# Performance work log

Measured on AMD Instinct MI355X. Metric: run time of the kernel, lower is better.

## Reference

```python
import jax, jax.numpy as jnp
import numpy as np


def setup_inputs() -> dict:
    key = jax.random.key(0)
    ks = jax.random.split(key, 6)
    B, F, C = 2048, 512, 64
    t_feat = jax.random.normal(ks[0], (B, F), dtype=jnp.float32)
    f_feat = jax.random.normal(ks[1], (B, F), dtype=jnp.float32)
    # proj Linear(F*F -> C); scale like torch default init (~1/sqrt(fan_in))
    W_proj = jax.random.normal(ks[2], (C, F * F), dtype=jnp.float32) / np.sqrt(F * F)
    b_proj = jnp.zeros((C,), dtype=jnp.float32)
    W1 = jax.random.normal(ks[3], (32, C), dtype=jnp.float32) / np.sqrt(C)
    b1 = jnp.zeros((32,), dtype=jnp.float32)
    W2 = jax.random.normal(ks[4], (1, 32), dtype=jnp.float32) / np.sqrt(32)
    b2 = jnp.zeros((1,), dtype=jnp.float32)
    return {"t_feat": t_feat, "f_feat": f_feat, "W_proj": W_proj, "b_proj": b_proj,
            "W1": W1, "b1": b1, "W2": W2, "b2": b2}


def reference(t_feat, f_feat, W_proj, b_proj, W1, b1, W2, b2):
    B, F = t_feat.shape
    C = W_proj.shape[0]
    # corr[b,i,j] = t[b,i] * f[b,j]; proj = corr_flat @ W_proj.T + b_proj.
    # Equivalent bilinear form computed WITHOUT materializing the (B,F,F) outer product:
    Wr = W_proj.reshape(C, F, F)            # W_proj[c, i*F + j] -> Wr[c,i,j]
    tmp = jnp.einsum('bi,cij->bcj', t_feat, Wr)   # (B, C, F)
    proj = jnp.einsum('bcj,bj->bc', tmp, f_feat) + b_proj  # (B, C)
    h = jax.nn.relu(proj)
    # GRL is identity in forward
    h2 = jax.nn.relu(h @ W1.T + b1)          # (B, 32)
    logit = h2 @ W2.T + b2                   # (B, 1)
    return logit
```

## Files before the change

kernel.cpp:

```cpp
#include <hip/hip_runtime.h>
#include <hip/hip_bf16.h>
#include <stdint.h>

#define BATCH 2048
#define FDIM 512
#define CDIM 64

typedef unsigned short ushort_t;
typedef __attribute__((ext_vector_type(8))) short short8;
typedef __attribute__((ext_vector_type(4))) float f32x4;

__device__ __forceinline__ ushort_t f2bf(float x) {
    union { float f; uint32_t u; } v; v.f = x;
    uint32_t u = v.u;
    uint32_t r = u + 0x7FFFu + ((u >> 16) & 1u);
    return (ushort_t)(r >> 16);
}

__global__ void convert_kernel(const float* __restrict__ src, ushort_t* __restrict__ dst) {
    int idx = blockIdx.x * 256 + threadIdx.x;
    float4 v = ((const float4*)src)[idx];
    ushort_t p[4] = { f2bf(v.x), f2bf(v.y), f2bf(v.z), f2bf(v.w) };
    *(uint2*)&dst[idx * 4] = *(uint2*)p;
}

#define AS3(p) ((__attribute__((address_space(3))) void*)(p))
#define AS1(p) ((const __attribute__((address_space(1))) void*)(p))

__launch_bounds__(256, 2)
__global__ void gemm_fused_kernel(const ushort_t* __restrict__ f16,
                                  const ushort_t* __restrict__ Wb,
                                  const float* __restrict__ t_feat,
                                  float* __restrict__ part) {
    __shared__ ushort_t As[128 * 32];
    __shared__ ushort_t Bs[128 * 32];
    __shared__ float scratch[256];

    const int tid  = threadIdx.x;
    const int wave = tid >> 6;
    const int lane = tid & 63;
    const int l15  = lane & 15;
    const int lg   = lane >> 4;

    const int b0 = blockIdx.x * 128;
    const int n0 = blockIdx.y * 128;

    const int m_base = (wave >> 1) * 64;
    const int nh     = wave & 1;
    const int n_base = nh * 64;

    f32x4 acc[4][4];
    #pragma unroll
    for (int mi = 0; mi < 4; mi++)
        #pragma unroll
        for (int ni = 0; ni < 4; ni++)
            acc[mi][ni] = (f32x4){0.f, 0.f, 0.f, 0.f};

    const int p    = tid >> 2;
    const int cph  = tid & 3;
    const int cg   = cph ^ ((p >> 1) & 3);
    const int nrot = ((p & 15) << 2) | (p >> 4);

    const ushort_t* gA0 = f16 + (size_t)(b0 + p) * FDIM + cg * 8;
    const ushort_t* gA1 = f16 + (size_t)(b0 + 64 + p) * FDIM + cg * 8;
    const ushort_t* gB0 = Wb + (size_t)(n0 + nrot) * FDIM + cg * 8;
    const ushort_t* gB1 = Wb + (size_t)(n0 + 64 + nrot) * FDIM + cg * 8;

    for (int k0 = 0; k0 < FDIM; k0 += 32) {
        __builtin_amdgcn_global_load_lds(AS1(gA0 + k0), AS3(&As[0 * 2048 + wave * 512]), 16, 0, 0);
        __builtin_amdgcn_global_load_lds(AS1(gA1 + k0), AS3(&As[1 * 2048 + wave * 512]), 16, 0, 0);
        __builtin_amdgcn_global_load_lds(AS1(gB0 + k0), AS3(&Bs[0 * 2048 + wave * 512]), 16, 0, 0);
        __builtin_amdgcn_global_load_lds(AS1(gB1 + k0), AS3(&Bs[1 * 2048 + wave * 512]), 16, 0, 0);
        __syncthreads();

        short8 a[4], b[4];
        #pragma unroll
        for (int mi = 0; mi < 4; mi++) {
            int r = m_base + mi * 16 + l15;
            a[mi] = *(const short8*)&As[r * 32 + (lg ^ ((r >> 1) & 3)) * 8];
        }
        #pragma unroll
        for (int ni = 0; ni < 4; ni++) {
            int q = n_base + ni * 16 + l15;
            b[ni] = *(const short8*)&Bs[q * 32 + (lg ^ ((q >> 1) & 3)) * 8];
        }

        #pragma unroll
        for (int mi = 0; mi < 4; mi++)
            #pragma unroll
            for (int ni = 0; ni < 4; ni++)
                acc[mi][ni] = __builtin_amdgcn_mfma_f32_16x16x32_bf16(a[mi], b[ni], acc[mi][ni], 0, 0, 0);

        __syncthreads();
    }

    const int c  = n0 >> 9;
    const int iq = (n0 >> 7) & 3;
    const int i_base = (n0 & 511) + n_base + l15 * 4;

    #pragma unroll
    for (int mi = 0; mi < 4; mi++) {
        #pragma unroll
        for (int r = 0; r < 4; r++) {
            int b_idx = b0 + m_base + mi * 16 + lg * 4 + r;
            const float4 tv = *(const float4*)&t_feat[(size_t)b_idx * FDIM + i_base];
            float s = acc[mi][0][r] * tv.x + acc[mi][1][r] * tv.y
                    + acc[mi][2][r] * tv.z + acc[mi][3][r] * tv.w;
            s += __shfl_xor(s, 1, 64);
            s += __shfl_xor(s, 2, 64);
            s += __shfl_xor(s, 4, 64);
            s += __shfl_xor(s, 8, 64);
            if (l15 == 0)
                scratch[(m_base + mi * 16 + lg * 4 + r) * 2 + nh] = s;
        }
    }
    __syncthreads();
    if (tid < 128) {
        float v = scratch[tid * 2] + scratch[tid * 2 + 1];
        part[(((size_t)(b0 + tid)) * 64 + c) * 4 + iq] = v;
    }
}

__global__ void mlp_kernel(const float* __restrict__ part,
                           const float* __restrict__ b_proj,
                           const float* __restrict__ W1, const float* __restrict__ b1,
                           const float* __restrict__ W2, const float* __restrict__ b2,
                           float* __restrict__ out) {
    int b = blockIdx.x * 64 + threadIdx.x;
    float h[64];
    const float4* p4 = (const float4*)&part[(size_t)b * 256];
    #pragma unroll
    for (int c = 0; c < 64; c++) {
        float4 v = p4[c];
        float s = v.x + v.y + v.z + v.w + b_proj[c];
        h[c] = s > 0.f ? s : 0.f;
    }
    float logit = b2[0];
    for (int o = 0; o < 32; o++) {
        float s = b1[o];
        #pragma unroll
        for (int c = 0; c < 64; c++) s += h[c] * W1[o * 64 + c];
        logit += (s > 0.f ? s : 0.f) * W2[o];
    }
    out[b] = logit;
}

extern "C" void kernel_launch(void* const* d_in, const int* in_sizes, int n_in,
                              void* d_out, int out_size, void* d_ws, size_t ws_size,
                              hipStream_t stream) {
    const float* t_feat = (const float*)d_in[0];
    const float* f_feat = (const float*)d_in[1];
    const float* W_proj = (const float*)d_in[2];
    const float* b_proj = (const float*)d_in[3];
    const float* W1     = (const float*)d_in[4];
    const float* b1     = (const float*)d_in[5];
    const float* W2     = (const float*)d_in[6];
    const float* b2     = (const float*)d_in[7];
    float* out = (float*)d_out;

    uint8_t* ws = (uint8_t*)d_ws;
    ushort_t* Wb   = (ushort_t*)(ws);
    ushort_t* f16  = (ushort_t*)(ws + 33554432);
    float*    part = (float*)(ws + 33554432 + 2097152);

    convert_kernel<<<dim3((CDIM * FDIM * FDIM) / 1024), dim3(256), 0, stream>>>(W_proj, Wb);
    convert_kernel<<<dim3((BATCH * FDIM) / 1024), dim3(256), 0, stream>>>(f_feat, f16);

    gemm_fused_kernel<<<dim3(BATCH / 128, (CDIM * FDIM) / 128), dim3(256), 0, stream>>>(
        f16, Wb, t_feat, part);

    mlp_kernel<<<dim3(BATCH / 64), dim3(64), 0, stream>>>(part, b_proj, W1, b1, W2, b2, out);
}
```

Measured before the change: 231.5 us.

## Double GEMM K-tile, remap blocks per XCD, widen convert, parallelize MLP

```diff
diff --git a/kernel.cpp b/kernel.cpp
--- a/kernel.cpp
+++ b/kernel.cpp
@@ -19,9 +19,11 @@
 
 __global__ void convert_kernel(const float* __restrict__ src, ushort_t* __restrict__ dst) {
     int idx = blockIdx.x * 256 + threadIdx.x;
-    float4 v = ((const float4*)src)[idx];
-    ushort_t p[4] = { f2bf(v.x), f2bf(v.y), f2bf(v.z), f2bf(v.w) };
-    *(uint2*)&dst[idx * 4] = *(uint2*)p;
+    float4 v0 = ((const float4*)src)[idx * 2];
+    float4 v1 = ((const float4*)src)[idx * 2 + 1];
+    ushort_t p[8] = { f2bf(v0.x), f2bf(v0.y), f2bf(v0.z), f2bf(v0.w),
+                      f2bf(v1.x), f2bf(v1.y), f2bf(v1.z), f2bf(v1.w) };
+    *(uint4*)&dst[idx * 8] = *(uint4*)p;
 }
 
 #define AS3(p) ((__attribute__((address_space(3))) void*)(p))
@@ -32,8 +34,8 @@
                                   const ushort_t* __restrict__ Wb,
                                   const float* __restrict__ t_feat,
                                   float* __restrict__ part) {
-    __shared__ ushort_t As[128 * 32];
-    __shared__ ushort_t Bs[128 * 32];
+    __shared__ ushort_t As[128 * 64];
+    __shared__ ushort_t Bs[128 * 64];
     __shared__ float scratch[256];
 
     const int tid  = threadIdx.x;
@@ -42,8 +44,11 @@
     const int l15  = lane & 15;
     const int lg   = lane >> 4;
 
-    const int b0 = blockIdx.x * 128;
-    const int n0 = blockIdx.y * 128;
+    const int g   = blockIdx.x + (blockIdx.y << 4);
+    const int xcd = g & 7;
+    const int s   = g >> 3;
+    const int b0  = (s & 15) << 7;
+    const int n0  = (xcd * 32 + (s >> 4)) << 7;
 
     const int m_base = (wave >> 1) * 64;
     const int nh     = wave & 1;
@@ -56,41 +61,49 @@
         for (int ni = 0; ni < 4; ni++)
             acc[mi][ni] = (f32x4){0.f, 0.f, 0.f, 0.f};
 
-    const int p    = tid >> 2;
-    const int cph  = tid & 3;
-    const int cg   = cph ^ ((p >> 1) & 3);
-    const int nrot = ((p & 15) << 2) | (p >> 4);
+    const ushort_t* srcA[4];
+    const ushort_t* srcB[4];
+    #pragma unroll
+    for (int q = 0; q < 4; q++) {
+        int seg  = wave * 4 + q;
+        int prow = seg * 8 + (lane >> 3);
+        int pch  = lane & 7;
+        int gch  = pch ^ (prow & 7);
+        srcA[q] = f16 + (size_t)(b0 + prow) * FDIM + gch * 8;
+        int grow = (prow & 64) | ((prow & 15) << 2) | ((prow >> 4) & 3);
+        srcB[q] = Wb + (size_t)(n0 + grow) * FDIM + gch * 8;
+    }
 
-    const ushort_t* gA0 = f16 + (size_t)(b0 + p) * FDIM + cg * 8;
-    const ushort_t* gA1 = f16 + (size_t)(b0 + 64 + p) * FDIM + cg * 8;
-    const ushort_t* gB0 = Wb + (size_t)(n0 + nrot) * FDIM + cg * 8;
-    const ushort_t* gB1 = Wb + (size_t)(n0 + 64 + nrot) * FDIM + cg * 8;
-
-    for (int k0 = 0; k0 < FDIM; k0 += 32) {
-        __builtin_amdgcn_global_load_lds(AS1(gA0 + k0), AS3(&As[0 * 2048 + wave * 512]), 16, 0, 0);
-        __builtin_amdgcn_global_load_lds(AS1(gA1 + k0), AS3(&As[1 * 2048 + wave * 512]), 16, 0, 0);
-        __builtin_amdgcn_global_load_lds(AS1(gB0 + k0), AS3(&Bs[0 * 2048 + wave * 512]), 16, 0, 0);
-        __builtin_amdgcn_global_load_lds(AS1(gB1 + k0), AS3(&Bs[1 * 2048 + wave * 512]), 16, 0, 0);
+    for (int k0 = 0; k0 < FDIM; k0 += 64) {
+        #pragma unroll
+        for (int q = 0; q < 4; q++) {
+            int seg = wave * 4 + q;
+            __builtin_amdgcn_global_load_lds(AS1(srcA[q] + k0), AS3(&As[seg * 512]), 16, 0, 0);
+            __builtin_amdgcn_global_load_lds(AS1(srcB[q] + k0), AS3(&Bs[seg * 512]), 16, 0, 0);
+        }
         __syncthreads();
 
-        short8 a[4], b[4];
         #pragma unroll
-        for (int mi = 0; mi < 4; mi++) {
-            int r = m_base + mi * 16 + l15;
-            a[mi] = *(const short8*)&As[r * 32 + (lg ^ ((r >> 1) & 3)) * 8];
+        for (int w = 0; w < 2; w++) {
+            short8 a[4], b[4];
+            #pragma unroll
+            for (int mi = 0; mi < 4; mi++) {
+                int r  = m_base + mi * 16 + l15;
+                int pc = (w * 4 + lg) ^ (r & 7);
+                a[mi] = *(const short8*)&As[r * 64 + pc * 8];
+            }
+            #pragma unroll
+            for (int ni = 0; ni < 4; ni++) {
+                int q2 = n_base + ni * 16 + l15;
+                int pc = (w * 4 + lg) ^ (q2 & 7);
+                b[ni] = *(const short8*)&Bs[q2 * 64 + pc * 8];
+            }
+            #pragma unroll
+            for (int mi = 0; mi < 4; mi++)
+                #pragma unroll
+                for (int ni = 0; ni < 4; ni++)
+                    acc[mi][ni] = __builtin_amdgcn_mfma_f32_16x16x32_bf16(a[mi], b[ni], acc[mi][ni], 0, 0, 0);
         }
-        #pragma unroll
-        for (int ni = 0; ni < 4; ni++) {
-            int q = n_base + ni * 16 + l15;
-            b[ni] = *(const short8*)&Bs[q * 32 + (lg ^ ((q >> 1) & 3)) * 8];
-        }
-
-        #pragma unroll
-        for (int mi = 0; mi < 4; mi++)
-            #pragma unroll
-            for (int ni = 0; ni < 4; ni++)
-                acc[mi][ni] = __builtin_amdgcn_mfma_f32_16x16x32_bf16(a[mi], b[ni], acc[mi][ni], 0, 0, 0);
-
         __syncthreads();
     }
 
@@ -104,14 +117,14 @@
         for (int r = 0; r < 4; r++) {
             int b_idx = b0 + m_base + mi * 16 + lg * 4 + r;
             const float4 tv = *(const float4*)&t_feat[(size_t)b_idx * FDIM + i_base];
-            float s = acc[mi][0][r] * tv.x + acc[mi][1][r] * tv.y
-                    + acc[mi][2][r] * tv.z + acc[mi][3][r] * tv.w;
-            s += __shfl_xor(s, 1, 64);
-            s += __shfl_xor(s, 2, 64);
-            s += __shfl_xor(s, 4, 64);
-            s += __shfl_xor(s, 8, 64);
+            float sv = acc[mi][0][r] * tv.x + acc[mi][1][r] * tv.y
+                     + acc[mi][2][r] * tv.z + acc[mi][3][r] * tv.w;
+            sv += __shfl_xor(sv, 1, 64);
+            sv += __shfl_xor(sv, 2, 64);
+            sv += __shfl_xor(sv, 4, 64);
+            sv += __shfl_xor(sv, 8, 64);
             if (l15 == 0)
-                scratch[(m_base + mi * 16 + lg * 4 + r) * 2 + nh] = s;
+                scratch[(m_base + mi * 16 + lg * 4 + r) * 2 + nh] = sv;
         }
     }
     __syncthreads();
@@ -126,23 +139,30 @@
                            const float* __restrict__ W1, const float* __restrict__ b1,
                            const float* __restrict__ W2, const float* __restrict__ b2,
                            float* __restrict__ out) {
-    int b = blockIdx.x * 64 + threadIdx.x;
-    float h[64];
-    const float4* p4 = (const float4*)&part[(size_t)b * 256];
+    __shared__ float h[8][64];
+    const int tid = threadIdx.x;
+    const int bl  = tid >> 5;
+    const int o   = tid & 31;
+    const int b   = blockIdx.x * 8 + bl;
+
     #pragma unroll
-    for (int c = 0; c < 64; c++) {
-        float4 v = p4[c];
-        float s = v.x + v.y + v.z + v.w + b_proj[c];
-        h[c] = s > 0.f ? s : 0.f;
+    for (int c = o; c < 64; c += 32) {
+        float4 v = *(const float4*)&part[(((size_t)b * 64 + c)) * 4];
+        float sv = v.x + v.y + v.z + v.w + b_proj[c];
+        h[bl][c] = sv > 0.f ? sv : 0.f;
     }
-    float logit = b2[0];
-    for (int o = 0; o < 32; o++) {
-        float s = b1[o];
-        #pragma unroll
-        for (int c = 0; c < 64; c++) s += h[c] * W1[o * 64 + c];
-        logit += (s > 0.f ? s : 0.f) * W2[o];
-    }
-    out[b] = logit;
+    __syncthreads();
+
+    float sv = b1[o];
+    #pragma unroll
+    for (int c = 0; c < 64; c++) sv += h[bl][c] * W1[o * 64 + c];
+    float v = (sv > 0.f ? sv : 0.f) * W2[o];
+    v += __shfl_xor(v, 1, 32);
+    v += __shfl_xor(v, 2, 32);
+    v += __shfl_xor(v, 4, 32);
+    v += __shfl_xor(v, 8, 32);
+    v += __shfl_xor(v, 16, 32);
+    if (o == 0) out[b] = v + b2[0];
 }
 
 extern "C" void kernel_launch(void* const* d_in, const int* in_sizes, int n_in,
@@ -163,11 +183,11 @@
     ushort_t* f16  = (ushort_t*)(ws + 33554432);
     float*    part = (float*)(ws + 33554432 + 2097152);
 
-    convert_kernel<<<dim3((CDIM * FDIM * FDIM) / 1024), dim3(256), 0, stream>>>(W_proj, Wb);
-    convert_kernel<<<dim3((BATCH * FDIM) / 1024), dim3(256), 0, stream>>>(f_feat, f16);
+    convert_kernel<<<dim3((CDIM * FDIM * FDIM) / 2048), dim3(256), 0, stream>>>(W_proj, Wb);
+    convert_kernel<<<dim3((BATCH * FDIM) / 2048), dim3(256), 0, stream>>>(f_feat, f16);
 
     gemm_fused_kernel<<<dim3(BATCH / 128, (CDIM * FDIM) / 128), dim3(256), 0, stream>>>(
         f16, Wb, t_feat, part);
 
-    mlp_kernel<<<dim3(BATCH / 64), dim3(64), 0, stream>>>(part, b_proj, W1, b1, W2, b2, out);
+    mlp_kernel<<<dim3(BATCH / 8), dim3(256), 0, stream>>>(part, b_proj, W1, b1, W2, b2, out);
 }
```

Result: faster. 217.1 us (-6.2%).
